# Optimization experiments

Measured on AMD Instinct MI355X. Metric: run time of the kernel, lower is better.

## Reference

```python
import jax, jax.numpy as jnp
import numpy as np

N = 20000   # atoms
E = 320000  # edges (avg degree 16)
H = 128     # hidden_channels / num_filters
G = 128     # num_gaussians
L = 4       # num_interactions
B = 200     # molecules
V = 80      # _MAX_ATOM_TYPE
CUT = 5.0
LOG2 = float(np.log(2.0))


def setup_inputs() -> dict:
    key = jax.random.key(0)
    ks = jax.random.split(key, 20)
    s = 0.05
    pos = jax.random.uniform(ks[0], (N, 3), dtype=jnp.float32) * 2.5  # dists < 5 = cutoff
    z = jax.random.randint(ks[1], (N,), 0, V)
    batch = jnp.sort(jax.random.randint(ks[2], (N,), 0, B))
    row = jax.random.randint(ks[3], (E,), 0, N)
    off = jax.random.randint(ks[4], (E,), 1, N)
    col = (row + off) % N  # guarantee row != col (no zero distances)
    edge_index = jnp.stack([row, col], axis=0)
    return {
        'pos': pos, 'z': z, 'batch': batch, 'edge_index': edge_index,
        'emb': jax.random.normal(ks[5], (V, H), jnp.float32) * s,
        'mlp_w1': jax.random.normal(ks[6], (L, G, H), jnp.float32) * s,
        'mlp_b1': jnp.zeros((L, H), jnp.float32),
        'mlp_w2': jax.random.normal(ks[7], (L, H, H), jnp.float32) * s,
        'mlp_b2': jnp.zeros((L, H), jnp.float32),
        'conv_lin1_w': jax.random.normal(ks[8], (L, H, H), jnp.float32) * s,
        'conv_lin2_w': jax.random.normal(ks[9], (L, H, H), jnp.float32) * s,
        'conv_lin2_b': jnp.zeros((L, H), jnp.float32),
        'blk_lin_w': jax.random.normal(ks[10], (L, H, H), jnp.float32) * s,
        'blk_lin_b': jnp.zeros((L, H), jnp.float32),
        'head_w1': jax.random.normal(ks[11], (H, H // 2), jnp.float32) * s,
        'head_b1': jnp.zeros((H // 2,), jnp.float32),
        'head_w2': jax.random.normal(ks[12], (H // 2, 1), jnp.float32) * s,
        'head_b2': jnp.zeros((1,), jnp.float32),
    }


def _ssp(x):  # ShiftedSoftplus
    return jax.nn.softplus(x) - LOG2


def _energy(pos, emb, mlp_w1, mlp_b1, mlp_w2, mlp_b2, conv_lin1_w, conv_lin2_w,
            conv_lin2_b, blk_lin_w, blk_lin_b, head_w1, head_b1, head_w2, head_b2,
            z, batch, edge_index):
    row, col = edge_index[0], edge_index[1]
    diff = pos[row] - pos[col]
    d = jnp.sqrt(jnp.sum(diff * diff, axis=-1))  # [E]
    # GaussianSmearing(0, cutoff, G)
    offset = jnp.linspace(0.0, CUT, G, dtype=pos.dtype)
    coeff = -0.5 / (offset[1] - offset[0]) ** 2
    edge_attr = jnp.exp(coeff * (d[:, None] - offset[None, :]) ** 2)  # [E,G]
    Ccut = 0.5 * (jnp.cos(d * jnp.pi / CUT) + 1.0)  # [E]
    h = emb[z]  # [N,H]
    for i in range(L):
        # per-edge filter MLP * cosine cutoff
        W = _ssp(edge_attr @ mlp_w1[i] + mlp_b1[i]) @ mlp_w2[i] + mlp_b2[i]
        W = W * Ccut[:, None]  # [E,H]
        hx = h @ conv_lin1_w[i]  # lin1, no bias
        msg = hx[row] * W  # gather x_j * filter
        agg = jax.ops.segment_sum(msg, col, num_segments=N)  # scatter-add
        v = agg @ conv_lin2_w[i] + conv_lin2_b[i]
        h = h + (_ssp(v) @ blk_lin_w[i] + blk_lin_b[i])  # residual InteractionBlock
    hh = _ssp(h @ head_w1 + head_b1) @ head_w2 + head_b2  # [N,1]
    return jax.ops.segment_sum(hh[:, 0], batch, num_segments=B)  # [B]


def reference(pos, z, batch, edge_index, emb, mlp_w1, mlp_b1, mlp_w2, mlp_b2,
              conv_lin1_w, conv_lin2_w, conv_lin2_b, blk_lin_w, blk_lin_b,
              head_w1, head_b1, head_w2, head_b2):
    args = (emb, mlp_w1, mlp_b1, mlp_w2, mlp_b2, conv_lin1_w, conv_lin2_w,
            conv_lin2_b, blk_lin_w, blk_lin_b, head_w1, head_b1, head_w2, head_b2)
    out = _energy(pos, *args, z, batch, edge_index)
    # forces = -d(sum(energy))/d(pos), matching torch.autograd.grad with ones grad_outputs
    forces = -jax.grad(lambda p: jnp.sum(_energy(p, *args, z, batch, edge_index)))(pos)
    return out, forces
```

## Files before the change

kernel.cpp:

```cpp
#include <hip/hip_runtime.h>

#define HD 128

constexpr int N_ATOMS = 20000;
constexpr int N_EDGES = 320000;
constexpr int NLAY   = 4;
constexpr int NMOL   = 200;
constexpr float FCUT  = 5.0f;
constexpr float DELTA = FCUT / 127.0f;
constexpr float GCOEFF = -0.5f / (DELTA * DELTA);
constexpr float PI_F  = 3.14159265358979323846f;
constexpr float LN2F  = 0.6931471805599453f;

typedef unsigned short u16;
typedef __attribute__((ext_vector_type(8))) short short8v;
typedef __attribute__((ext_vector_type(4))) float f32x4;

__device__ __forceinline__ float sspf(float x) {
  return fmaxf(x, 0.0f) + log1pf(expf(-fabsf(x))) - LN2F;
}
__device__ __forceinline__ float sigmf(float x) {
  return 1.0f / (1.0f + expf(-x));
}

__device__ __forceinline__ unsigned bfpack(float a, float b) {
  unsigned ua = __float_as_uint(a);
  unsigned ub = __float_as_uint(b);
  ua = (ua + 0x7FFFu + ((ua >> 16) & 1u)) >> 16;
  ub = (ub + 0x7FFFu + ((ub >> 16) & 1u)) >> 16;
  return (ub << 16) | ua;
}
__device__ __forceinline__ float bflo(unsigned p) { return __uint_as_float(p << 16); }
__device__ __forceinline__ float bfhi(unsigned p) { return __uint_as_float(p & 0xFFFF0000u); }
__device__ __forceinline__ u16 f2bf(float x) {
  unsigned u = __float_as_uint(x);
  u = (u + 0x7FFFu + ((u >> 16) & 1u)) >> 16;
  return (u16)u;
}
__device__ __forceinline__ float bf2f(u16 b) { return __uint_as_float((unsigned)b << 16); }

__device__ __forceinline__ unsigned packhl(float s) {
  unsigned hs = __float_as_uint(s) & 0xffff0000u;
  float lo = s - __uint_as_float(hs);
  return hs | (__float_as_uint(lo) >> 16);
}

__device__ __forceinline__ unsigned hpair_f32(unsigned a, unsigned b, unsigned& lopair) {
  unsigned ha = a & 0xffff0000u, hb = b & 0xffff0000u;
  float la = __uint_as_float(a) - __uint_as_float(ha);
  float lb = __uint_as_float(b) - __uint_as_float(hb);
  lopair = (__float_as_uint(lb) & 0xffff0000u) | (__float_as_uint(la) >> 16);
  return hb | (ha >> 16);
}


__global__ __launch_bounds__(256) void h0_k(
    const float* __restrict__ emb, const int* __restrict__ z,
    float* __restrict__ h0)
{
  int i = blockIdx.x * 256 + threadIdx.x;
  if (i >= N_ATOMS * HD) return;
  int n = i >> 7, k = i & 127;
  h0[i] = emb[z[n] * HD + k];
}

__global__ __launch_bounds__(256) void wprep_k(
    const float* __restrict__ l1, const float* __restrict__ l2,
    const float* __restrict__ bw, const float* __restrict__ mw1,
    const float* __restrict__ mw2,
    u16* __restrict__ wt, u16* __restrict__ wp, u16* __restrict__ mt)
{
  int i = blockIdx.x * 256 + threadIdx.x;
  if (i >= NLAY * 5 * HD * HD) return;
  int e = i & (HD * HD - 1);
  int wl = i >> 14;
  int wsel = wl % 5;
  int lay = wl / 5;
  const float* W;
  if      (wsel == 0) W = l1;
  else if (wsel == 1) W = l2;
  else if (wsel == 2) W = bw;
  else if (wsel == 3) W = mw1;
  else                W = mw2;
  W += (size_t)lay * HD * HD;
  u16 b = f2bf(W[e]);
  int k = e >> 7, n = e & 127;
  if (wsel < 3) {
    size_t base = (size_t)(lay * 3 + wsel) << 14;
    wp[base + e] = b;
    wt[base + (size_t)n * HD + k] = b;
  } else {
    size_t base = (size_t)(lay * 2 + (wsel - 3)) << 14;
    mt[base + (size_t)n * HD + k] = b;
  }
}

__global__ __launch_bounds__(256) void histboth_k(
    const int* __restrict__ row, const int* __restrict__ col,
    int* __restrict__ cntR, int* __restrict__ cntC)
{
  int e = blockIdx.x * 256 + threadIdx.x;
  if (e >= N_EDGES) return;
  atomicAdd(&cntC[col[e]], 1);
  atomicAdd(&cntR[row[e]], 1);
}

__global__ __launch_bounds__(256) void scan2_k(
    const int* __restrict__ cnt0, const int* __restrict__ cnt1,
    int* __restrict__ cptr, int* __restrict__ rptr,
    int* __restrict__ cur0, int* __restrict__ cur1)
{
  constexpr int CH = 80;
  __shared__ int part[256];
  const int* cnt = blockIdx.x == 0 ? cnt0 : cnt1;
  int* ptr = blockIdx.x == 0 ? cptr : rptr;
  int* cur = blockIdx.x == 0 ? cur0 : cur1;
  int t = threadIdx.x;
  int base = t * CH;
  int v[CH];
  if (base + CH <= N_ATOMS) {
#pragma unroll
    for (int i = 0; i < CH / 4; i++) {
      int4 q = *(const int4*)(cnt + base + i * 4);
      v[4*i+0] = q.x; v[4*i+1] = q.y; v[4*i+2] = q.z; v[4*i+3] = q.w;
    }
  } else {
#pragma unroll
    for (int i = 0; i < CH; i++)
      v[i] = (base + i < N_ATOMS) ? cnt[base + i] : 0;
  }
  int s = 0;
#pragma unroll
  for (int i = 0; i < CH; i++) s += v[i];
  part[t] = s;
  __syncthreads();
  for (int off = 1; off < 256; off <<= 1) {
    int u = (t >= off) ? part[t - off] : 0;
    __syncthreads();
    part[t] += u;
    __syncthreads();
  }
  int run = part[t] - s;
#pragma unroll
  for (int i = 0; i < CH; i++) {
    int idx = base + i;
    if (idx < N_ATOMS) { ptr[idx] = run; cur[idx] = run; }
    else if (idx == N_ATOMS) ptr[idx] = run;
    run += v[i];
  }
}

__global__ __launch_bounds__(256) void scatboth_k(
    const float* __restrict__ pos, const int* __restrict__ row,
    const int* __restrict__ col, int* __restrict__ cur0,
    int* __restrict__ cur1, unsigned* __restrict__ cpk,
    unsigned* __restrict__ rpk, float* __restrict__ cdist,
    float* __restrict__ rdist, float4* __restrict__ ccoef,
    float4* __restrict__ rcoefA, float4* __restrict__ rcoefB,
    int* __restrict__ cslot, float inv_h, float hstep)
{
  int e = blockIdx.x * 256 + threadIdx.x;
  if (e >= N_EDGES) return;
  int r = row[e], c = col[e];
  float dx = pos[3*r+0] - pos[3*c+0];
  float dy = pos[3*r+1] - pos[3*c+1];
  float dz = pos[3*r+2] - pos[3*c+2];
  float d = sqrtf(dx*dx + dy*dy + dz*dz);
  float fi = d * inv_h;
  int i0 = (int)fi;
  float t = fi - (float)i0;
  float t2 = t * t, t3 = t2 * t;
  float a00 = 2.f*t3 - 3.f*t2 + 1.f;
  float a10 = (t3 - 2.f*t2 + t) * hstep;
  float a01 = 3.f*t2 - 2.f*t3;
  float a11 = (t3 - t2) * hstep;
  float b00 = (6.f*t2 - 6.f*t) * inv_h;
  float b10 = 3.f*t2 - 4.f*t + 1.f;
  float b01 = -b00;
  float b11 = 3.f*t2 - 2.f*t;
  int pr = atomicAdd(&cur1[r], 1);
  rpk[pr] = (unsigned)c | ((unsigned)i0 << 16);
  rdist[pr] = d;
  rcoefA[pr] = make_float4(a00, a10, a01, a11);
  rcoefB[pr] = make_float4(b00, b10, b01, b11);
  int pc = atomicAdd(&cur0[c], 1);
  cpk[pc] = (unsigned)r | ((unsigned)i0 << 16);
  cdist[pc] = d;
  ccoef[pc] = make_float4(a00, a10, a01, a11);
  cslot[pc] = pr;
}

__global__ __launch_bounds__(256) void nodeA_k(
    float* __restrict__ A, float* __restrict__ dA, int nnode, float hstep)
{
  int i = blockIdx.x * 256 + threadIdx.x;
  if (i >= nnode * HD) return;
  int node = i >> 7, g = i & 127;
  float d = (float)node * hstep;
  float t = d - (float)g * DELTA;
  float a = expf(GCOEFF * t * t);
  A[i] = a;
  dA[i] = a * 2.0f * GCOEFF * t;
}

__global__ __launch_bounds__(256) void nodeact_k(
    const float* __restrict__ t1, const float* __restrict__ u,
    float* __restrict__ s, float* __restrict__ sp, int total)
{
  int i = blockIdx.x * 256 + threadIdx.x;
  if (i >= total) return;
  float x = t1[i];
  s[i] = sspf(x);
  sp[i] = sigmf(x) * u[i];
}

__global__ __launch_bounds__(256) void nodecomb_k(
    const float* __restrict__ P0, const float* __restrict__ D0,
    unsigned* __restrict__ T, int nnode, float hstep)
{
  int i = blockIdx.x * 256 + threadIdx.x;
  int total = NLAY * nnode * HD;
  if (i >= total) return;
  int rem = i % (nnode * HD);
  int node = rem >> 7;
  float d = (float)node * hstep;
  float C  = 0.5f * cosf(d * (PI_F / FCUT)) + 0.5f;
  float Cp = -0.5f * sinf(d * (PI_F / FCUT)) * (PI_F / FCUT);
  float p = P0[i], q = D0[i];
  T[i] = bfpack(p * C, q * C + p * Cp);
}

__device__ __forceinline__ void wave_mm(
    const float* __restrict__ Av, const u16* __restrict__ Bt,
    int m0, int wbase, int lc, int lg, int mclamp, f32x4 acc[2])
{
  short8v bfr[4][2];
#pragma unroll
  for (int ks = 0; ks < 4; ++ks)
#pragma unroll
    for (int nt = 0; nt < 2; ++nt)
      bfr[ks][nt] = *(const short8v*)(Bt + (size_t)(wbase + nt*16 + lc) * HD + ks*32 + lg*8);
  int ar = m0 + lc;
  if (ar > mclamp) ar = mclamp;
  f32x4 z = {0.f, 0.f, 0.f, 0.f};
  acc[0] = z; acc[1] = z;
#pragma unroll
  for (int ks = 0; ks < 4; ++ks) {
    const float* p = Av + (size_t)ar * HD + ks*32 + lg*8;
    uint4 u0 = *(const uint4*)p;
    uint4 u1 = *(const uint4*)(p + 4);
    unsigned p0l, p1l, p2l, p3l;
    unsigned p0h = hpair_f32(u0.x, u0.y, p0l);
    unsigned p1h = hpair_f32(u0.z, u0.w, p1l);
    unsigned p2h = hpair_f32(u1.x, u1.y, p2l);
    unsigned p3h = hpair_f32(u1.z, u1.w, p3l);
    uint4 hv = make_uint4(p0h, p1h, p2h, p3h);
    uint4 lv = make_uint4(p0l, p1l, p2l, p3l);
    short8v ah = *(short8v*)&hv, al = *(short8v*)&lv;
    acc[0] = __builtin_amdgcn_mfma_f32_16x16x32_bf16(ah, bfr[ks][0], acc[0], 0, 0, 0);
    acc[1] = __builtin_amdgcn_mfma_f32_16x16x32_bf16(ah, bfr[ks][1], acc[1], 0, 0, 0);
    acc[0] = __builtin_amdgcn_mfma_f32_16x16x32_bf16(al, bfr[ks][0], acc[0], 0, 0, 0);
    acc[1] = __builtin_amdgcn_mfma_f32_16x16x32_bf16(al, bfr[ks][1], acc[1], 0, 0, 0);
  }
}

__device__ __forceinline__ void wave_mm_lds(
    const unsigned (*__restrict__ Sl)[132], const u16* __restrict__ Bt,
    int wbase, int lc, int lg, f32x4 acc[2])
{
  short8v bfr[4][2];
#pragma unroll
  for (int ks = 0; ks < 4; ++ks)
#pragma unroll
    for (int nt = 0; nt < 2; ++nt)
      bfr[ks][nt] = *(const short8v*)(Bt + (size_t)(wbase + nt*16 + lc) * HD + ks*32 + lg*8);
  f32x4 z = {0.f, 0.f, 0.f, 0.f};
  acc[0] = z; acc[1] = z;
#pragma unroll
  for (int ks = 0; ks < 4; ++ks) {
    uint4 u0 = *(const uint4*)&Sl[lc][ks*32 + lg*8];
    uint4 u1 = *(const uint4*)&Sl[lc][ks*32 + lg*8 + 4];
    uint4 hv = make_uint4(
      (u0.y & 0xffff0000u) | (u0.x >> 16),
      (u0.w & 0xffff0000u) | (u0.z >> 16),
      (u1.y & 0xffff0000u) | (u1.x >> 16),
      (u1.w & 0xffff0000u) | (u1.z >> 16));
    uint4 lv = make_uint4(
      (u0.y << 16) | (u0.x & 0xffffu),
      (u0.w << 16) | (u0.z & 0xffffu),
      (u1.y << 16) | (u1.x & 0xffffu),
      (u1.w << 16) | (u1.z & 0xffffu));
    short8v ah = *(short8v*)&hv, al = *(short8v*)&lv;
    acc[0] = __builtin_amdgcn_mfma_f32_16x16x32_bf16(ah, bfr[ks][0], acc[0], 0, 0, 0);
    acc[1] = __builtin_amdgcn_mfma_f32_16x16x32_bf16(ah, bfr[ks][1], acc[1], 0, 0, 0);
    acc[0] = __builtin_amdgcn_mfma_f32_16x16x32_bf16(al, bfr[ks][0], acc[0], 0, 0, 0);
    acc[1] = __builtin_amdgcn_mfma_f32_16x16x32_bf16(al, bfr[ks][1], acc[1], 0, 0, 0);
  }
}

__global__ __launch_bounds__(256) void nmm_hx_k(
    const float* __restrict__ h, const u16* __restrict__ Bt,
    u16* __restrict__ hx, int M)
{
  int t = threadIdx.x, lane = t & 63;
  int lc = lane & 15, lg = lane >> 4;
  int wbase = (t >> 6) * 32;
  int m0 = blockIdx.x * 16;
  f32x4 acc[2];
  wave_mm(h, Bt, m0, wbase, lc, lg, M - 1, acc);
#pragma unroll
  for (int nt = 0; nt < 2; ++nt) {
    int ccol = wbase + nt*16 + lc;
#pragma unroll
    for (int j = 0; j < 4; ++j) {
      int grow = m0 + lg*4 + j;
      if (grow < M) hx[(size_t)grow * HD + ccol] = f2bf(acc[nt][j]);
    }
  }
}

__global__ __launch_bounds__(256) void nmm_bwdT_k(
    const float* __restrict__ A, const u16* __restrict__ Bp,
    const float* __restrict__ addin, float* __restrict__ C, int M)
{
  int t = threadIdx.x, lane = t & 63;
  int lc = lane & 15, lg = lane >> 4;
  int wbase = (t >> 6) * 32;
  int m0 = blockIdx.x * 16;
  f32x4 acc[2];
  wave_mm(A, Bp, m0, wbase, lc, lg, M - 1, acc);
#pragma unroll
  for (int nt = 0; nt < 2; ++nt) {
    int ccol = wbase + nt*16 + lc;
#pragma unroll
    for (int j = 0; j < 4; ++j) {
      int grow = m0 + lg*4 + j;
      if (grow < M)
        C[(size_t)grow * HD + ccol] = acc[nt][j] + addin[(size_t)grow * HD + ccol];
    }
  }
}

__global__ __launch_bounds__(256) void ftail_f_k(
    const float* __restrict__ agg, const u16* __restrict__ l2t,
    const float* __restrict__ l2b, const u16* __restrict__ bwt,
    const float* __restrict__ bb, const float* __restrict__ h,
    u16* __restrict__ svb, float* __restrict__ hout,
    const u16* __restrict__ l1n, u16* __restrict__ hxn, int M)
{
  __shared__ unsigned Sl[16][132];
  int t = threadIdx.x, lane = t & 63;
  int lc = lane & 15, lg = lane >> 4;
  int wbase = (t >> 6) * 32;
  int m0 = blockIdx.x * 16;
  f32x4 acc[2];
  wave_mm(agg, l2t, m0, wbase, lc, lg, M - 1, acc);
#pragma unroll
  for (int nt = 0; nt < 2; ++nt) {
    int ccol = wbase + nt*16 + lc;
    float bv = l2b[ccol];
#pragma unroll
    for (int j = 0; j < 4; ++j) {
      int lrow = lg*4 + j;
      int grow = m0 + lrow;
      float s = 0.0f;
      if (grow < M) {
        float x = acc[nt][j] + bv;
        svb[(size_t)grow * HD + ccol] = f2bf(sigmf(x));
        s = sspf(x);
      }
      Sl[lrow][ccol] = packhl(s);
    }
  }
  __syncthreads();
  wave_mm_lds(Sl, bwt, wbase, lc, lg, acc);

  float ho[2][4];
#pragma unroll
  for (int nt = 0; nt < 2; ++nt) {
    int ccol = wbase + nt*16 + lc;
    float bv = bb[ccol];
#pragma unroll
    for (int j = 0; j < 4; ++j) {
      int grow = m0 + lg*4 + j;
      float x = 0.0f;
      if (grow < M) {
        x = acc[nt][j] + bv + h[(size_t)grow * HD + ccol];
        hout[(size_t)grow * HD + ccol] = x;
      }
      ho[nt][j] = x;
    }
  }
  if (l1n) {
    __syncthreads();
#pragma unroll
    for (int nt = 0; nt < 2; ++nt) {
      int ccol = wbase + nt*16 + lc;
#pragma unroll
      for (int j = 0; j < 4; ++j)
        Sl[lg*4 + j][ccol] = packhl(ho[nt][j]);
    }
    __syncthreads();
    wave_mm_lds(Sl, l1n, wbase, lc, lg, acc);
#pragma unroll
    for (int nt = 0; nt < 2; ++nt) {
      int ccol = wbase + nt*16 + lc;
#pragma unroll
      for (int j = 0; j < 4; ++j) {
        int grow = m0 + lg*4 + j;
        if (grow < M) hxn[(size_t)grow * HD + ccol] = f2bf(acc[nt][j]);
      }
    }
  }
}

__global__ __launch_bounds__(256) void bhead_f_k(
    const float* __restrict__ g, const u16* __restrict__ bwp,
    const u16* __restrict__ svb, const u16* __restrict__ l2p,
    u16* __restrict__ dagg, int M)
{
  __shared__ unsigned Sl[16][132];
  int t = threadIdx.x, lane = t & 63;
  int lc = lane & 15, lg = lane >> 4;
  int wbase = (t >> 6) * 32;
  int m0 = blockIdx.x * 16;
  f32x4 acc[2];
  wave_mm(g, bwp, m0, wbase, lc, lg, M - 1, acc);
#pragma unroll
  for (int nt = 0; nt < 2; ++nt) {
    int ccol = wbase + nt*16 + lc;
#pragma unroll
    for (int j = 0; j < 4; ++j) {
      int lrow = lg*4 + j;
      int grow = m0 + lrow;
      float dv = 0.0f;
      if (grow < M)
        dv = acc[nt][j] * bf2f(svb[(size_t)grow * HD + ccol]);
      Sl[lrow][ccol] = packhl(dv);
    }
  }
  __syncthreads();
  wave_mm_lds(Sl, l2p, wbase, lc, lg, acc);
#pragma unroll
  for (int nt = 0; nt < 2; ++nt) {
    int ccol = wbase + nt*16 + lc;
#pragma unroll
    for (int j = 0; j < 4; ++j) {
      int grow = m0 + lg*4 + j;
      if (grow < M) dagg[(size_t)grow * HD + ccol] = f2bf(acc[nt][j]);
    }
  }
}

__global__ __launch_bounds__(256) void tblmm2_k(
    const float* __restrict__ A0, const float* __restrict__ A1, size_t astride,
    const u16* __restrict__ Bt, size_t bstride,
    const float* __restrict__ bias0, size_t biasstride,
    float* __restrict__ C0, float* __restrict__ C1, size_t cstride, int M)
{
  int l = blockIdx.y;
  int zz = blockIdx.z;
  const float* A = (zz ? A1 : A0) + (size_t)l * astride;
  const u16* B = Bt + (size_t)l * bstride;
  const float* bias = zz ? nullptr : (bias0 ? bias0 + (size_t)l * biasstride : nullptr);
  float* C = (zz ? C1 : C0) + (size_t)l * cstride;
  int t = threadIdx.x, lane = t & 63;
  int lc = lane & 15, lg = lane >> 4;
  int wbase = (t >> 6) * 32;
  int m0 = blockIdx.x * 16;
  f32x4 acc[2];
  wave_mm(A, B, m0, wbase, lc, lg, M - 1, acc);
#pragma unroll
  for (int nt = 0; nt < 2; ++nt) {
    int ccol = wbase + nt*16 + lc;
    float bv = bias ? bias[ccol] : 0.0f;
#pragma unroll
    for (int j = 0; j < 4; ++j) {
      int grow = m0 + lg*4 + j;
      if (grow < M) C[(size_t)grow * HD + ccol] = acc[nt][j] + bv;
    }
  }
}

__global__ __launch_bounds__(256) void gath_fwd_k(
    const int* __restrict__ cptr, const unsigned* __restrict__ cpk,
    const float4* __restrict__ ccoef, const unsigned* __restrict__ T,
    const unsigned* __restrict__ hx, float* __restrict__ agg)
{
  int a = blockIdx.x * 4 + (threadIdx.x >> 6);
  if (a >= N_ATOMS) return;
  int half = (threadIdx.x >> 5) & 1;
  int l32 = threadIdx.x & 31;
  int ch = l32 * 4;
  int beg = cptr[a], end = cptr[a + 1];
  float s0 = 0.f, s1 = 0.f, s2 = 0.f, s3 = 0.f;
#pragma unroll 2
  for (int j = beg + half; j < end; j += 2) {
    unsigned pk = cpk[j];
    float4 cf = ccoef[j];
    int other = pk & 0xffffu;
    const unsigned* tp = T + (size_t)(pk >> 16) * HD + ch;
    uint4 q0 = *(const uint4*)(tp);
    uint4 q1 = *(const uint4*)(tp + HD);
    uint2 hp = *(const uint2*)(hx + (size_t)other * 64 + l32 * 2);
    float v0 = cf.x*bflo(q0.x) + cf.y*bfhi(q0.x) + cf.z*bflo(q1.x) + cf.w*bfhi(q1.x);
    float v1 = cf.x*bflo(q0.y) + cf.y*bfhi(q0.y) + cf.z*bflo(q1.y) + cf.w*bfhi(q1.y);
    float v2 = cf.x*bflo(q0.z) + cf.y*bfhi(q0.z) + cf.z*bflo(q1.z) + cf.w*bfhi(q1.z);
    float v3 = cf.x*bflo(q0.w) + cf.y*bfhi(q0.w) + cf.z*bflo(q1.w) + cf.w*bfhi(q1.w);
    s0 = fmaf(bflo(hp.x), v0, s0);
    s1 = fmaf(bfhi(hp.x), v1, s1);
    s2 = fmaf(bflo(hp.y), v2, s2);
    s3 = fmaf(bfhi(hp.y), v3, s3);
  }
  s0 += __shfl_xor(s0, 32, 64);
  s1 += __shfl_xor(s1, 32, 64);
  s2 += __shfl_xor(s2, 32, 64);
  s3 += __shfl_xor(s3, 32, 64);
  if (half == 0)
    *(float4*)(agg + (size_t)a * HD + ch) = make_float4(s0, s1, s2, s3);
}

__global__ __launch_bounds__(256) void gath_bwd_k(
    const int* __restrict__ rptr, const unsigned* __restrict__ rpk,
    const float4* __restrict__ rcoefA, const float4* __restrict__ rcoefB,
    const unsigned* __restrict__ T, const unsigned* __restrict__ dagg,
    const unsigned* __restrict__ hx, float* __restrict__ dhx,
    float* __restrict__ ddslot, int accum)
{
  int a = blockIdx.x * 4 + (threadIdx.x >> 6);
  if (a >= N_ATOMS) return;
  int half = (threadIdx.x >> 5) & 1;
  int l32 = threadIdx.x & 31;
  int ch = l32 * 4;
  int beg = rptr[a], end = rptr[a + 1];
  uint2 hp = *(const uint2*)(hx + (size_t)a * 64 + l32 * 2);
  float h0 = bflo(hp.x), h1 = bfhi(hp.x), h2 = bflo(hp.y), h3 = bfhi(hp.y);
  float s0 = 0.f, s1 = 0.f, s2 = 0.f, s3 = 0.f;
#pragma unroll 2
  for (int j = beg + half; j < end; j += 2) {
    unsigned pk = rpk[j];
    float4 ca = rcoefA[j];
    float4 cb = rcoefB[j];
    int other = pk & 0xffffu;
    const unsigned* tp = T + (size_t)(pk >> 16) * HD + ch;
    uint4 q0 = *(const uint4*)(tp);
    uint4 q1 = *(const uint4*)(tp + HD);
    uint2 dp = *(const uint2*)(dagg + (size_t)other * 64 + l32 * 2);
    float da0 = bflo(dp.x), da1 = bfhi(dp.x), da2 = bflo(dp.y), da3 = bfhi(dp.y);
    float x0l = bflo(q0.x), x0h = bfhi(q0.x), y0l = bflo(q1.x), y0h = bfhi(q1.x);
    float x1l = bflo(q0.y), x1h = bfhi(q0.y), y1l = bflo(q1.y), y1h = bfhi(q1.y);
    float x2l = bflo(q0.z), x2h = bfhi(q0.z), y2l = bflo(q1.z), y2h = bfhi(q1.z);
    float x3l = bflo(q0.w), x3h = bfhi(q0.w), y3l = bflo(q1.w), y3h = bfhi(q1.w);
    float v0 = ca.x*x0l + ca.y*x0h + ca.z*y0l + ca.w*y0h;
    float v1 = ca.x*x1l + ca.y*x1h + ca.z*y1l + ca.w*y1h;
    float v2 = ca.x*x2l + ca.y*x2h + ca.z*y2l + ca.w*y2h;
    float v3 = ca.x*x3l + ca.y*x3h + ca.z*y3l + ca.w*y3h;
    float g0 = cb.x*x0l + cb.y*x0h + cb.z*y0l + cb.w*y0h;
    float g1 = cb.x*x1l + cb.y*x1h + cb.z*y1l + cb.w*y1h;
    float g2 = cb.x*x2l + cb.y*x2h + cb.z*y2l + cb.w*y2h;
    float g3 = cb.x*x3l + cb.y*x3h + cb.z*y3l + cb.w*y3h;
    s0 = fmaf(da0, v0, s0);
    s1 = fmaf(da1, v1, s1);
    s2 = fmaf(da2, v2, s2);
    s3 = fmaf(da3, v3, s3);
    float dot = da0*h0*g0 + da1*h1*g1 + da2*h2*g2 + da3*h3*g3;
#pragma unroll
    for (int off = 16; off > 0; off >>= 1) dot += __shfl_down(dot, off, 32);
    if (l32 == 0) ddslot[j] = accum ? (ddslot[j] + dot) : dot;
  }
  s0 += __shfl_xor(s0, 32, 64);
  s1 += __shfl_xor(s1, 32, 64);
  s2 += __shfl_xor(s2, 32, 64);
  s3 += __shfl_xor(s3, 32, 64);
  if (half == 0)
    *(float4*)(dhx + (size_t)a * HD + ch) = make_float4(s0, s1, s2, s3);
}

__global__ __launch_bounds__(256) void headf_k(
    const float* __restrict__ h4, const float* __restrict__ hw1,
    const float* __restrict__ hb1, const float* __restrict__ hw2,
    const float* __restrict__ hb2, float* __restrict__ ea,
    float* __restrict__ gh)
{
  __shared__ float As[16][68];
  __shared__ float Bs[16][132];
  __shared__ float Ss[64][68];
  __shared__ float red[64][17];
  int t = threadIdx.x;
  int tx = t & 15, ty = t >> 4;
  int m0 = blockIdx.x * 64;

  float acc4[4][4];
#pragma unroll
  for (int r = 0; r < 4; r++)
#pragma unroll
    for (int c = 0; c < 4; c++) acc4[r][c] = 0.0f;

  for (int k0 = 0; k0 < HD; k0 += 16) {
    {
      int rrow = t >> 2;
      int kg = (t & 3) * 4;
      int gm = m0 + rrow;
      float4 av = make_float4(0.f, 0.f, 0.f, 0.f);
      if (gm < N_ATOMS) av = *(const float4*)(h4 + (size_t)gm * HD + k0 + kg);
      As[kg+0][rrow] = av.x; As[kg+1][rrow] = av.y;
      As[kg+2][rrow] = av.z; As[kg+3][rrow] = av.w;
    }
    if (t < 256) {
      int kk = t >> 4;
      int n4 = (t & 15) * 4;
      float4 bv = *(const float4*)(hw1 + (size_t)(k0 + kk) * 64 + n4);
      *(float4*)&Bs[kk][n4] = bv;
    }
    __syncthreads();
#pragma unroll
    for (int kk = 0; kk < 16; kk++) {
      float a[4], b[4];
#pragma unroll
      for (int r = 0; r < 4; r++) a[r] = As[kk][ty * 4 + r];
#pragma unroll
      for (int c = 0; c < 4; c++) b[c] = Bs[kk][tx * 4 + c];
#pragma unroll
      for (int r = 0; r < 4; r++)
#pragma unroll
        for (int c = 0; c < 4; c++) acc4[r][c] = fmaf(a[r], b[c], acc4[r][c]);
    }
    __syncthreads();
  }

  {
    int n0 = tx * 4;
    float b1v[4], w2v[4];
#pragma unroll
    for (int c = 0; c < 4; c++) { b1v[c] = hb1[n0 + c]; w2v[c] = hw2[n0 + c]; }
#pragma unroll
    for (int r = 0; r < 4; r++) {
      int lr = ty * 4 + r;
      float p = 0.0f;
#pragma unroll
      for (int c = 0; c < 4; c++) {
        float x = acc4[r][c] + b1v[c];
        p += sspf(x) * w2v[c];
        Ss[lr][n0 + c] = sigmf(x) * w2v[c];
      }
      red[lr][tx] = p;
    }
  }
  __syncthreads();
  if (t < 64) {
    int gm = m0 + t;
    if (gm < N_ATOMS) {
      float s = hb2[0];
#pragma unroll
      for (int j = 0; j < 16; j++) s += red[t][j];
      ea[gm] = s;
    }
  }

  float acc[4][8];
#pragma unroll
  for (int r = 0; r < 4; r++)
#pragma unroll
    for (int c = 0; c < 8; c++) acc[r][c] = 0.0f;

  for (int j0 = 0; j0 < 64; j0 += 16) {
#pragma unroll
    for (int it = 0; it < 2; it++) {
      int idx = t + it * 256;
      int n = idx >> 2;
      int jg = (idx & 3) * 4;
      float4 bv = *(const float4*)(hw1 + (size_t)n * 64 + j0 + jg);
      Bs[jg+0][n] = bv.x; Bs[jg+1][n] = bv.y;
      Bs[jg+2][n] = bv.z; Bs[jg+3][n] = bv.w;
    }
    __syncthreads();
#pragma unroll
    for (int kk = 0; kk < 16; kk++) {
      float a[4], b[8];
#pragma unroll
      for (int r = 0; r < 4; r++) a[r] = Ss[ty * 4 + r][j0 + kk];
#pragma unroll
      for (int c = 0; c < 8; c++) b[c] = Bs[kk][tx * 8 + c];
#pragma unroll
      for (int r = 0; r < 4; r++)
#pragma unroll
        for (int c = 0; c < 8; c++) acc[r][c] = fmaf(a[r], b[c], acc[r][c]);
    }
    __syncthreads();
  }

  int n0 = tx * 8;
#pragma unroll
  for (int r = 0; r < 4; r++) {
    int gm = m0 + ty * 4 + r;
    if (gm >= N_ATOMS) continue;
    *(float4*)(gh + (size_t)gm * HD + n0)     = *(float4*)&acc[r][0];
    *(float4*)(gh + (size_t)gm * HD + n0 + 4) = *(float4*)&acc[r][4];
  }
}

__global__ __launch_bounds__(64) void ered_k(
    const int* __restrict__ batch, const float* __restrict__ ea,
    float* __restrict__ energy)
{
  int m = blockIdx.x;
  int lo = 0, hi = N_ATOMS;
  while (lo < hi) { int mid = (lo + hi) >> 1; if (batch[mid] < m) lo = mid + 1; else hi = mid; }
  int beg = lo;
  lo = beg; hi = N_ATOMS;
  while (lo < hi) { int mid = (lo + hi) >> 1; if (batch[mid] < m + 1) lo = mid + 1; else hi = mid; }
  int end = lo;
  float s = 0.0f;
  for (int i = beg + threadIdx.x; i < end; i += 64) s += ea[i];
#pragma unroll
  for (int off = 32; off > 0; off >>= 1) s += __shfl_down(s, off, 64);
  if (threadIdx.x == 0) energy[m] = s;
}

__global__ __launch_bounds__(256) void forceg_k(
    const int* __restrict__ rptr, const unsigned* __restrict__ rpk,
    const float* __restrict__ rdist,
    const int* __restrict__ cptr, const unsigned* __restrict__ cpk,
    const float* __restrict__ cdist, const int* __restrict__ cslot,
    const float* __restrict__ ddslot, const float* __restrict__ pos,
    float* __restrict__ force)
{
  int idx = blockIdx.x * 256 + threadIdx.x;
  int a = idx >> 3;
  int g = idx & 7;
  if (a >= N_ATOMS) return;
  float px = pos[3*a+0], py = pos[3*a+1], pz = pos[3*a+2];
  float fx = 0.f, fy = 0.f, fz = 0.f;
  int beg = rptr[a], end = rptr[a+1];
  for (int j = beg + g; j < end; j += 8) {
    int o = rpk[j] & 0xffffu;
    float w = ddslot[j] / rdist[j];
    fx -= w * (px - pos[3*o+0]);
    fy -= w * (py - pos[3*o+1]);
    fz -= w * (pz - pos[3*o+2]);
  }
  beg = cptr[a]; end = cptr[a+1];
  for (int j = beg + g; j < end; j += 8) {
    int o = cpk[j] & 0xffffu;
    float w = ddslot[cslot[j]] / cdist[j];
    fx -= w * (px - pos[3*o+0]);
    fy -= w * (py - pos[3*o+1]);
    fz -= w * (pz - pos[3*o+2]);
  }
#pragma unroll
  for (int off = 4; off > 0; off >>= 1) {
    fx += __shfl_down(fx, off, 8);
    fy += __shfl_down(fy, off, 8);
    fz += __shfl_down(fz, off, 8);
  }
  if (g == 0) {
    force[3*a+0] = fx;
    force[3*a+1] = fy;
    force[3*a+2] = fz;
  }
}

static inline int nblk(int m) { return (m + 63) / 64; }

extern "C" void kernel_launch(void* const* d_in, const int* in_sizes, int n_in,
                              void* d_out, int out_size, void* d_ws, size_t ws_size,
                              hipStream_t stream)
{
  const float* pos   = (const float*)d_in[0];
  const int*   z     = (const int*)d_in[1];
  const int*   batch = (const int*)d_in[2];
  const int*   eidx  = (const int*)d_in[3];
  const float* emb   = (const float*)d_in[4];
  const float* mlp_w1 = (const float*)d_in[5];
  const float* mlp_b1 = (const float*)d_in[6];
  const float* mlp_w2 = (const float*)d_in[7];
  const float* mlp_b2 = (const float*)d_in[8];
  const float* lin1_w = (const float*)d_in[9];
  const float* lin2_w = (const float*)d_in[10];
  const float* lin2_b = (const float*)d_in[11];
  const float* blk_w  = (const float*)d_in[12];
  const float* blk_b  = (const float*)d_in[13];
  const float* hw1 = (const float*)d_in[14];
  const float* hb1 = (const float*)d_in[15];
  const float* hw2 = (const float*)d_in[16];
  const float* hb2 = (const float*)d_in[17];

  float* out = (float*)d_out;
  float* ws  = (float*)d_ws;

  const int* row = eidx;
  const int* col = eidx + N_EDGES;

  const size_t NH = (size_t)N_ATOMS * HD;
  size_t o = 0;
  float* ddslot = ws + o; o += N_EDGES;
  int* cptr = (int*)(ws + o); o += N_ATOMS + 1;
  int* rptr = (int*)(ws + o); o += N_ATOMS + 1;
  int* cnt0 = (int*)(ws + o); o += N_ATOMS;
  int* cnt1 = (int*)(ws + o); o += N_ATOMS;
  int* cur0 = (int*)(ws + o); o += N_ATOMS;
  int* cur1 = (int*)(ws + o); o += N_ATOMS;
  unsigned* cpk = (unsigned*)(ws + o); o += N_EDGES;
  unsigned* rpk = (unsigned*)(ws + o); o += N_EDGES;
  int* cslot = (int*)(ws + o); o += N_EDGES;
  float* cdist = ws + o; o += N_EDGES;
  float* rdist = ws + o; o += N_EDGES;
  o = (o + 3) & ~(size_t)3;
  float4* ccoef  = (float4*)(ws + o); o += (size_t)4 * N_EDGES;
  float4* rcoefA = (float4*)(ws + o); o += (size_t)4 * N_EDGES;
  float4* rcoefB = (float4*)(ws + o); o += (size_t)4 * N_EDGES;
  u16* wt = (u16*)(ws + o); o += (size_t)NLAY * 3 * HD * HD / 2;
  u16* wp = (u16*)(ws + o); o += (size_t)NLAY * 3 * HD * HD / 2;
  u16* mt = (u16*)(ws + o); o += (size_t)NLAY * 2 * HD * HD / 2;
  float* hxb[4];
  for (int i = 0; i < 4; i++) { hxb[i] = ws + o; o += NH / 2; }
  float* svb[4];
  for (int i = 0; i < 4; i++) { svb[i] = ws + o; o += NH / 2; }
  float* hA  = ws + o; o += NH;
  float* hB  = ws + o; o += NH;
  float* agg = ws + o; o += NH;
  float* g0b = ws + o; o += NH;
  float* g1b = ws + o; o += NH;
  float* dgb = ws + o; o += NH / 2;

  int NT = 1024;
  while (NT > 128) {
    size_t need = o + (size_t)NLAY * (NT + 1) * HD;
    if (need * sizeof(float) <= ws_size) break;
    NT >>= 1;
  }
  const int NN = NT + 1;
  const float hstep = FCUT / (float)NT;
  const float inv_h = (float)NT / FCUT;
  unsigned* T = (unsigned*)(ws + o); o += (size_t)NLAY * NN * HD;

  const int EB = (N_EDGES + 255) / 256;

  hipMemsetAsync(cnt0, 0, 2 * N_ATOMS * sizeof(int), stream);

  wprep_k<<<(NLAY * 5 * HD * HD + 255) / 256, 256, 0, stream>>>(
      lin1_w, lin2_w, blk_w, mlp_w1, mlp_w2, wt, wp, mt);

  histboth_k<<<EB, 256, 0, stream>>>(row, col, cnt1, cnt0);
  scan2_k<<<2, 256, 0, stream>>>(cnt0, cnt1, cptr, rptr, cur0, cur1);
  scatboth_k<<<EB, 256, 0, stream>>>(pos, row, col, cur0, cur1, cpk, rpk,
                                     cdist, rdist, ccoef, rcoefA, rcoefB,
                                     cslot, inv_h, hstep);

  {
    const size_t LNH = (size_t)NN * HD;
    float* Anode  = agg;
    float* dAnode = agg + LNH;
    float* t1 = dgb;
    float* u  = g0b;
    float* s  = g1b;
    float* sp = hA;
    nodeA_k<<<((int)LNH + 255) / 256, 256, 0, stream>>>(Anode, dAnode, NN, hstep);
    dim3 gB16((NN + 15) / 16, NLAY, 2);
    tblmm2_k<<<gB16, 256, 0, stream>>>(Anode, dAnode, 0, mt, 32768,
                                       mlp_b1, HD, t1, u, LNH, NN);
    int tot = (int)(NLAY * LNH);
    nodeact_k<<<(tot + 255) / 256, 256, 0, stream>>>(t1, u, s, sp, tot);
    float* P0 = dgb;
    float* D0 = g0b;
    tblmm2_k<<<gB16, 256, 0, stream>>>(s, sp, LNH, mt + 16384, 32768,
                                       mlp_b2, HD, P0, D0, LNH, NN);
    nodecomb_k<<<(tot + 255) / 256, 256, 0, stream>>>(P0, D0, T, NN, hstep);
  }

  h0_k<<<(N_ATOMS * HD + 255) / 256, 256, 0, stream>>>(emb, z, hA);

  const int AB = (N_ATOMS + 3) / 4;
  const int GB = nblk(N_ATOMS);
  const int NB16 = (N_ATOMS + 15) / 16;

  float* hcur = hA;
  float* hnxt = hB;
  nmm_hx_k<<<NB16, 256, 0, stream>>>(hcur, wt, (u16*)hxb[0], N_ATOMS);
  for (int i = 0; i < NLAY; i++) {
    const u16* l2t = wt + ((size_t)(i*3 + 1) << 14);
    const u16* bwt = wt + ((size_t)(i*3 + 2) << 14);
    const u16* l1n = (i < NLAY - 1) ? wt + ((size_t)((i+1)*3 + 0) << 14) : nullptr;
    u16* hxn = (i < NLAY - 1) ? (u16*)hxb[i+1] : nullptr;
    const float* l2bi = lin2_b + (size_t)i * HD;
    const float* bbi  = blk_b + (size_t)i * HD;
    const unsigned* Tl = T + (size_t)i * NN * HD;

    gath_fwd_k<<<AB, 256, 0, stream>>>(cptr, cpk, ccoef, Tl,
                                       (const unsigned*)hxb[i], agg);
    ftail_f_k<<<NB16, 256, 0, stream>>>(agg, l2t, l2bi, bwt, bbi, hcur,
                                        (u16*)svb[i], hnxt, l1n, hxn, N_ATOMS);
    float* tmp = hcur; hcur = hnxt; hnxt = tmp;
  }

  float* ea = dgb;
  headf_k<<<GB, 256, 0, stream>>>(hcur, hw1, hb1, hw2, hb2, ea, g0b);
  ered_k<<<NMOL, 64, 0, stream>>>(batch, ea, out);

  float* gcur = g0b;
  float* gnxt = g1b;
  for (int i = NLAY - 1; i >= 0; i--) {
    const u16* l1p = wp + ((size_t)(i*3 + 0) << 14);
    const u16* l2p = wp + ((size_t)(i*3 + 1) << 14);
    const u16* bwp = wp + ((size_t)(i*3 + 2) << 14);
    const unsigned* Tl = T + (size_t)i * NN * HD;

    bhead_f_k<<<NB16, 256, 0, stream>>>(gcur, bwp, (const u16*)svb[i], l2p,
                                        (u16*)dgb, N_ATOMS);
    gath_bwd_k<<<AB, 256, 0, stream>>>(rptr, rpk, rcoefA, rcoefB, Tl,
                                       (const unsigned*)dgb,
                                       (const unsigned*)hxb[i], agg, ddslot,
                                       i != NLAY - 1);
    if (i > 0) {
      nmm_bwdT_k<<<NB16, 256, 0, stream>>>(agg, l1p, gcur, gnxt, N_ATOMS);
      float* tmp = gcur; gcur = gnxt; gnxt = tmp;
    }
  }

  forceg_k<<<(N_ATOMS * 8 + 255) / 256, 256, 0, stream>>>(
      rptr, rpk, rdist, cptr, cpk, cdist, cslot, ddslot, pos, out + NMOL);
}
```

Before: 834.2 us.

## Recompute Hermite coefficients in gathers and process atoms in degree-sorted order

The edge scatter now stores only the packed index plus the fractional spline parameter t per edge, instead of precomputed float4 coefficient arrays. The gather kernels recompute the cubic Hermite weights and derivative weights from t on the fly. This cuts per-edge memory traffic at the cost of a few extra FLOPs per edge. A counting sort by atom degree, built from three new small kernels, supplies a permutation so that wavefronts in the gather kernels handle atoms of similar degree, reducing load imbalance. The permuted order may scatter output writes and adds launch overhead.

```diff
diff --git a/kernel.cpp b/kernel.cpp
--- a/kernel.cpp
+++ b/kernel.cpp
@@ -153,11 +153,9 @@
 __global__ __launch_bounds__(256) void scatboth_k(
     const float* __restrict__ pos, const int* __restrict__ row,
     const int* __restrict__ col, int* __restrict__ cur0,
-    int* __restrict__ cur1, unsigned* __restrict__ cpk,
-    unsigned* __restrict__ rpk, float* __restrict__ cdist,
-    float* __restrict__ rdist, float4* __restrict__ ccoef,
-    float4* __restrict__ rcoefA, float4* __restrict__ rcoefB,
-    int* __restrict__ cslot, float inv_h, float hstep)
+    int* __restrict__ cur1, uint2* __restrict__ cpk2,
+    uint2* __restrict__ rpk2, float* __restrict__ cdist,
+    float* __restrict__ rdist, int* __restrict__ cslot, float inv_h)
 {
   int e = blockIdx.x * 256 + threadIdx.x;
   if (e >= N_EDGES) return;
@@ -169,25 +167,60 @@
   float fi = d * inv_h;
   int i0 = (int)fi;
   float t = fi - (float)i0;
-  float t2 = t * t, t3 = t2 * t;
-  float a00 = 2.f*t3 - 3.f*t2 + 1.f;
-  float a10 = (t3 - 2.f*t2 + t) * hstep;
-  float a01 = 3.f*t2 - 2.f*t3;
-  float a11 = (t3 - t2) * hstep;
-  float b00 = (6.f*t2 - 6.f*t) * inv_h;
-  float b10 = 3.f*t2 - 4.f*t + 1.f;
-  float b01 = -b00;
-  float b11 = 3.f*t2 - 2.f*t;
+  unsigned pk = (unsigned)c | ((unsigned)i0 << 16);
+  unsigned tu = __float_as_uint(t);
   int pr = atomicAdd(&cur1[r], 1);
-  rpk[pr] = (unsigned)c | ((unsigned)i0 << 16);
+  rpk2[pr] = make_uint2(pk, tu);
   rdist[pr] = d;
-  rcoefA[pr] = make_float4(a00, a10, a01, a11);
-  rcoefB[pr] = make_float4(b00, b10, b01, b11);
   int pc = atomicAdd(&cur0[c], 1);
-  cpk[pc] = (unsigned)r | ((unsigned)i0 << 16);
+  cpk2[pc] = make_uint2((unsigned)r | ((unsigned)i0 << 16), tu);
   cdist[pc] = d;
-  ccoef[pc] = make_float4(a00, a10, a01, a11);
   cslot[pc] = pr;
+}
+
+__global__ __launch_bounds__(256) void dhist_k(
+    const int* __restrict__ cptr, const int* __restrict__ rptr,
+    int* __restrict__ binc, int* __restrict__ binr)
+{
+  int a = blockIdx.x * 256 + threadIdx.x;
+  if (a >= N_ATOMS) return;
+  int dc = cptr[a+1] - cptr[a];
+  int dr = rptr[a+1] - rptr[a];
+  atomicAdd(&binc[255 - min(dc, 255)], 1);
+  atomicAdd(&binr[255 - min(dr, 255)], 1);
+}
+
+__global__ __launch_bounds__(256) void dscan_k(
+    int* __restrict__ binc, int* __restrict__ binr)
+{
+  int* bin = blockIdx.x == 0 ? binc : binr;
+  __shared__ int sh[256];
+  int t = threadIdx.x;
+  int v = bin[t];
+  sh[t] = v;
+  __syncthreads();
+  for (int off = 1; off < 256; off <<= 1) {
+    int u = (t >= off) ? sh[t - off] : 0;
+    __syncthreads();
+    sh[t] += u;
+    __syncthreads();
+  }
+  bin[t] = sh[t] - v;
+}
+
+__global__ __launch_bounds__(256) void dscat_k(
+    const int* __restrict__ cptr, const int* __restrict__ rptr,
+    int* __restrict__ binc, int* __restrict__ binr,
+    int* __restrict__ permc, int* __restrict__ permr)
+{
+  int a = blockIdx.x * 256 + threadIdx.x;
+  if (a >= N_ATOMS) return;
+  int dc = cptr[a+1] - cptr[a];
+  int dr = rptr[a+1] - rptr[a];
+  int sc = atomicAdd(&binc[255 - min(dc, 255)], 1);
+  permc[sc] = a;
+  int sr = atomicAdd(&binr[255 - min(dr, 255)], 1);
+  permr[sr] = a;
 }
 
 __global__ __launch_bounds__(256) void nodeA_k(
@@ -483,12 +516,13 @@
 }
 
 __global__ __launch_bounds__(256) void gath_fwd_k(
-    const int* __restrict__ cptr, const unsigned* __restrict__ cpk,
-    const float4* __restrict__ ccoef, const unsigned* __restrict__ T,
-    const unsigned* __restrict__ hx, float* __restrict__ agg)
-{
-  int a = blockIdx.x * 4 + (threadIdx.x >> 6);
-  if (a >= N_ATOMS) return;
+    const int* __restrict__ perm, const int* __restrict__ cptr,
+    const uint2* __restrict__ cpk2, const unsigned* __restrict__ T,
+    const unsigned* __restrict__ hx, float* __restrict__ agg, float hstep)
+{
+  int ai = blockIdx.x * 4 + (threadIdx.x >> 6);
+  if (ai >= N_ATOMS) return;
+  int a = perm[ai];
   int half = (threadIdx.x >> 5) & 1;
   int l32 = threadIdx.x & 31;
   int ch = l32 * 4;
@@ -496,17 +530,22 @@
   float s0 = 0.f, s1 = 0.f, s2 = 0.f, s3 = 0.f;
 #pragma unroll 2
   for (int j = beg + half; j < end; j += 2) {
-    unsigned pk = cpk[j];
-    float4 cf = ccoef[j];
-    int other = pk & 0xffffu;
-    const unsigned* tp = T + (size_t)(pk >> 16) * HD + ch;
+    uint2 pk2 = cpk2[j];
+    float t = __uint_as_float(pk2.y);
+    int other = pk2.x & 0xffffu;
+    float t2 = t * t, t3 = t2 * t;
+    float cx = 2.f*t3 - 3.f*t2 + 1.f;
+    float cy = (t3 - 2.f*t2 + t) * hstep;
+    float cz = 3.f*t2 - 2.f*t3;
+    float cw = (t3 - t2) * hstep;
+    const unsigned* tp = T + (size_t)(pk2.x >> 16) * HD + ch;
     uint4 q0 = *(const uint4*)(tp);
     uint4 q1 = *(const uint4*)(tp + HD);
     uint2 hp = *(const uint2*)(hx + (size_t)other * 64 + l32 * 2);
-    float v0 = cf.x*bflo(q0.x) + cf.y*bfhi(q0.x) + cf.z*bflo(q1.x) + cf.w*bfhi(q1.x);
-    float v1 = cf.x*bflo(q0.y) + cf.y*bfhi(q0.y) + cf.z*bflo(q1.y) + cf.w*bfhi(q1.y);
-    float v2 = cf.x*bflo(q0.z) + cf.y*bfhi(q0.z) + cf.z*bflo(q1.z) + cf.w*bfhi(q1.z);
-    float v3 = cf.x*bflo(q0.w) + cf.y*bfhi(q0.w) + cf.z*bflo(q1.w) + cf.w*bfhi(q1.w);
+    float v0 = cx*bflo(q0.x) + cy*bfhi(q0.x) + cz*bflo(q1.x) + cw*bfhi(q1.x);
+    float v1 = cx*bflo(q0.y) + cy*bfhi(q0.y) + cz*bflo(q1.y) + cw*bfhi(q1.y);
+    float v2 = cx*bflo(q0.z) + cy*bfhi(q0.z) + cz*bflo(q1.z) + cw*bfhi(q1.z);
+    float v3 = cx*bflo(q0.w) + cy*bfhi(q0.w) + cz*bflo(q1.w) + cw*bfhi(q1.w);
     s0 = fmaf(bflo(hp.x), v0, s0);
     s1 = fmaf(bfhi(hp.x), v1, s1);
     s2 = fmaf(bflo(hp.y), v2, s2);
@@ -521,14 +560,15 @@
 }
 
 __global__ __launch_bounds__(256) void gath_bwd_k(
-    const int* __restrict__ rptr, const unsigned* __restrict__ rpk,
-    const float4* __restrict__ rcoefA, const float4* __restrict__ rcoefB,
-    const unsigned* __restrict__ T, const unsigned* __restrict__ dagg,
-    const unsigned* __restrict__ hx, float* __restrict__ dhx,
-    float* __restrict__ ddslot, int accum)
-{
-  int a = blockIdx.x * 4 + (threadIdx.x >> 6);
-  if (a >= N_ATOMS) return;
+    const int* __restrict__ perm, const int* __restrict__ rptr,
+    const uint2* __restrict__ rpk2, const unsigned* __restrict__ T,
+    const unsigned* __restrict__ dagg, const unsigned* __restrict__ hx,
+    float* __restrict__ dhx, float* __restrict__ ddslot, int accum,
+    float hstep, float inv_h)
+{
+  int ai = blockIdx.x * 4 + (threadIdx.x >> 6);
+  if (ai >= N_ATOMS) return;
+  int a = perm[ai];
   int half = (threadIdx.x >> 5) & 1;
   int l32 = threadIdx.x & 31;
   int ch = l32 * 4;
@@ -538,11 +578,19 @@
   float s0 = 0.f, s1 = 0.f, s2 = 0.f, s3 = 0.f;
 #pragma unroll 2
   for (int j = beg + half; j < end; j += 2) {
-    unsigned pk = rpk[j];
-    float4 ca = rcoefA[j];
-    float4 cb = rcoefB[j];
-    int other = pk & 0xffffu;
-    const unsigned* tp = T + (size_t)(pk >> 16) * HD + ch;
+    uint2 pk2 = rpk2[j];
+    float t = __uint_as_float(pk2.y);
+    int other = pk2.x & 0xffffu;
+    float t2 = t * t, t3 = t2 * t;
+    float cax = 2.f*t3 - 3.f*t2 + 1.f;
+    float cay = (t3 - 2.f*t2 + t) * hstep;
+    float caz = 3.f*t2 - 2.f*t3;
+    float caw = (t3 - t2) * hstep;
+    float cbx = (6.f*t2 - 6.f*t) * inv_h;
+    float cby = 3.f*t2 - 4.f*t + 1.f;
+    float cbz = -cbx;
+    float cbw = 3.f*t2 - 2.f*t;
+    const unsigned* tp = T + (size_t)(pk2.x >> 16) * HD + ch;
     uint4 q0 = *(const uint4*)(tp);
     uint4 q1 = *(const uint4*)(tp + HD);
     uint2 dp = *(const uint2*)(dagg + (size_t)other * 64 + l32 * 2);
@@ -551,14 +599,14 @@
     float x1l = bflo(q0.y), x1h = bfhi(q0.y), y1l = bflo(q1.y), y1h = bfhi(q1.y);
     float x2l = bflo(q0.z), x2h = bfhi(q0.z), y2l = bflo(q1.z), y2h = bfhi(q1.z);
     float x3l = bflo(q0.w), x3h = bfhi(q0.w), y3l = bflo(q1.w), y3h = bfhi(q1.w);
-    float v0 = ca.x*x0l + ca.y*x0h + ca.z*y0l + ca.w*y0h;
-    float v1 = ca.x*x1l + ca.y*x1h + ca.z*y1l + ca.w*y1h;
-    float v2 = ca.x*x2l + ca.y*x2h + ca.z*y2l + ca.w*y2h;
-    float v3 = ca.x*x3l + ca.y*x3h + ca.z*y3l + ca.w*y3h;
-    float g0 = cb.x*x0l + cb.y*x0h + cb.z*y0l + cb.w*y0h;
-    float g1 = cb.x*x1l + cb.y*x1h + cb.z*y1l + cb.w*y1h;
-    float g2 = cb.x*x2l + cb.y*x2h + cb.z*y2l + cb.w*y2h;
-    float g3 = cb.x*x3l + cb.y*x3h + cb.z*y3l + cb.w*y3h;
+    float v0 = cax*x0l + cay*x0h + caz*y0l + caw*y0h;
+    float v1 = cax*x1l + cay*x1h + caz*y1l + caw*y1h;
+    float v2 = cax*x2l + cay*x2h + caz*y2l + caw*y2h;
+    float v3 = cax*x3l + cay*x3h + caz*y3l + caw*y3h;
+    float g0 = cbx*x0l + cby*x0h + cbz*y0l + cbw*y0h;
+    float g1 = cbx*x1l + cby*x1h + cbz*y1l + cbw*y1h;
+    float g2 = cbx*x2l + cby*x2h + cbz*y2l + cbw*y2h;
+    float g3 = cbx*x3l + cby*x3h + cbz*y3l + cbw*y3h;
     s0 = fmaf(da0, v0, s0);
     s1 = fmaf(da1, v1, s1);
     s2 = fmaf(da2, v2, s2);
@@ -718,9 +766,9 @@
 }
 
 __global__ __launch_bounds__(256) void forceg_k(
-    const int* __restrict__ rptr, const unsigned* __restrict__ rpk,
+    const int* __restrict__ rptr, const uint2* __restrict__ rpk2,
     const float* __restrict__ rdist,
-    const int* __restrict__ cptr, const unsigned* __restrict__ cpk,
+    const int* __restrict__ cptr, const uint2* __restrict__ cpk2,
     const float* __restrict__ cdist, const int* __restrict__ cslot,
     const float* __restrict__ ddslot, const float* __restrict__ pos,
     float* __restrict__ force)
@@ -733,7 +781,7 @@
   float fx = 0.f, fy = 0.f, fz = 0.f;
   int beg = rptr[a], end = rptr[a+1];
   for (int j = beg + g; j < end; j += 8) {
-    int o = rpk[j] & 0xffffu;
+    int o = rpk2[j].x & 0xffffu;
     float w = ddslot[j] / rdist[j];
     fx -= w * (px - pos[3*o+0]);
     fy -= w * (py - pos[3*o+1]);
@@ -741,7 +789,7 @@
   }
   beg = cptr[a]; end = cptr[a+1];
   for (int j = beg + g; j < end; j += 8) {
-    int o = cpk[j] & 0xffffu;
+    int o = cpk2[j].x & 0xffffu;
     float w = ddslot[cslot[j]] / cdist[j];
     fx -= w * (px - pos[3*o+0]);
     fy -= w * (py - pos[3*o+1]);
@@ -798,17 +846,18 @@
   int* rptr = (int*)(ws + o); o += N_ATOMS + 1;
   int* cnt0 = (int*)(ws + o); o += N_ATOMS;
   int* cnt1 = (int*)(ws + o); o += N_ATOMS;
+  int* binc = (int*)(ws + o); o += 256;
+  int* binr = (int*)(ws + o); o += 256;
   int* cur0 = (int*)(ws + o); o += N_ATOMS;
   int* cur1 = (int*)(ws + o); o += N_ATOMS;
-  unsigned* cpk = (unsigned*)(ws + o); o += N_EDGES;
-  unsigned* rpk = (unsigned*)(ws + o); o += N_EDGES;
+  int* permc = (int*)(ws + o); o += N_ATOMS;
+  int* permr = (int*)(ws + o); o += N_ATOMS;
   int* cslot = (int*)(ws + o); o += N_EDGES;
   float* cdist = ws + o; o += N_EDGES;
   float* rdist = ws + o; o += N_EDGES;
-  o = (o + 3) & ~(size_t)3;
-  float4* ccoef  = (float4*)(ws + o); o += (size_t)4 * N_EDGES;
-  float4* rcoefA = (float4*)(ws + o); o += (size_t)4 * N_EDGES;
-  float4* rcoefB = (float4*)(ws + o); o += (size_t)4 * N_EDGES;
+  o = (o + 1) & ~(size_t)1;
+  uint2* cpk2 = (uint2*)(ws + o); o += (size_t)2 * N_EDGES;
+  uint2* rpk2 = (uint2*)(ws + o); o += (size_t)2 * N_EDGES;
   u16* wt = (u16*)(ws + o); o += (size_t)NLAY * 3 * HD * HD / 2;
   u16* wp = (u16*)(ws + o); o += (size_t)NLAY * 3 * HD * HD / 2;
   u16* mt = (u16*)(ws + o); o += (size_t)NLAY * 2 * HD * HD / 2;
@@ -835,17 +884,21 @@
   unsigned* T = (unsigned*)(ws + o); o += (size_t)NLAY * NN * HD;
 
   const int EB = (N_EDGES + 255) / 256;
-
-  hipMemsetAsync(cnt0, 0, 2 * N_ATOMS * sizeof(int), stream);
+  const int ABK = (N_ATOMS + 255) / 256;
+
+  hipMemsetAsync(cnt0, 0, (2 * N_ATOMS + 512) * sizeof(int), stream);
 
   wprep_k<<<(NLAY * 5 * HD * HD + 255) / 256, 256, 0, stream>>>(
       lin1_w, lin2_w, blk_w, mlp_w1, mlp_w2, wt, wp, mt);
 
   histboth_k<<<EB, 256, 0, stream>>>(row, col, cnt1, cnt0);
   scan2_k<<<2, 256, 0, stream>>>(cnt0, cnt1, cptr, rptr, cur0, cur1);
-  scatboth_k<<<EB, 256, 0, stream>>>(pos, row, col, cur0, cur1, cpk, rpk,
-                                     cdist, rdist, ccoef, rcoefA, rcoefB,
-                                     cslot, inv_h, hstep);
+  scatboth_k<<<EB, 256, 0, stream>>>(pos, row, col, cur0, cur1, cpk2, rpk2,
+                                     cdist, rdist, cslot, inv_h);
+
+  dhist_k<<<ABK, 256, 0, stream>>>(cptr, rptr, binc, binr);
+  dscan_k<<<2, 256, 0, stream>>>(binc, binr);
+  dscat_k<<<ABK, 256, 0, stream>>>(cptr, rptr, binc, binr, permc, permr);
 
   {
     const size_t LNH = (size_t)NN * HD;
@@ -886,8 +939,8 @@
     const float* bbi  = blk_b + (size_t)i * HD;
     const unsigned* Tl = T + (size_t)i * NN * HD;
 
-    gath_fwd_k<<<AB, 256, 0, stream>>>(cptr, cpk, ccoef, Tl,
-                                       (const unsigned*)hxb[i], agg);
+    gath_fwd_k<<<AB, 256, 0, stream>>>(permc, cptr, cpk2, Tl,
+                                       (const unsigned*)hxb[i], agg, hstep);
     ftail_f_k<<<NB16, 256, 0, stream>>>(agg, l2t, l2bi, bwt, bbi, hcur,
                                         (u16*)svb[i], hnxt, l1n, hxn, N_ATOMS);
     float* tmp = hcur; hcur = hnxt; hnxt = tmp;
@@ -907,10 +960,10 @@
 
     bhead_f_k<<<NB16, 256, 0, stream>>>(gcur, bwp, (const u16*)svb[i], l2p,
                                         (u16*)dgb, N_ATOMS);
-    gath_bwd_k<<<AB, 256, 0, stream>>>(rptr, rpk, rcoefA, rcoefB, Tl,
+    gath_bwd_k<<<AB, 256, 0, stream>>>(permr, rptr, rpk2, Tl,
                                        (const unsigned*)dgb,
                                        (const unsigned*)hxb[i], agg, ddslot,
-                                       i != NLAY - 1);
+                                       i != NLAY - 1, hstep, inv_h);
     if (i > 0) {
       nmm_bwdT_k<<<NB16, 256, 0, stream>>>(agg, l1p, gcur, gnxt, N_ATOMS);
       float* tmp = gcur; gcur = gnxt; gnxt = tmp;
@@ -918,5 +971,5 @@
   }
 
   forceg_k<<<(N_ATOMS * 8 + 255) / 256, 256, 0, stream>>>(
-      rptr, rpk, rdist, cptr, cpk, cdist, cslot, ddslot, pos, out + NMOL);
-}
+      rptr, rpk2, rdist, cptr, cpk2, cdist, cslot, ddslot, pos, out + NMOL);
+}
```

Result: slower. 911.5 us (+9.3%).
